# Kernel tuning notes

Hardware: AMD Instinct MI355X
Metric: run time of the kernel (lower is better)

The kernel has to match this reference:

```python
import jax, jax.numpy as jnp
import numpy as np

N, E, F_IN, C, D = 50000, 200000, 384, 384, 16
NEG_SLOPE = 0.2


def setup_inputs() -> dict:
    key = jax.random.key(0)
    ks = jax.random.split(key, 12)
    x = jax.random.normal(ks[0], (N, F_IN), jnp.float32)
    # random edges with no self-loops (PyG GATConv removes self loops before re-adding them)
    src = jax.random.randint(ks[1], (E,), 0, N)
    off = jax.random.randint(ks[2], (E,), 1, N)
    dst = (src + off) % N
    edge_index = jnp.stack([src, dst]).astype(jnp.int32)  # [2, E]
    edge_attr = jax.random.uniform(ks[3], (E, D), jnp.float32)
    # GATConv params (heads=1): lin (no bias), att_src/att_dst/att_edge, lin_edge (no bias), bias
    W_lin = jax.random.normal(ks[4], (F_IN, C), jnp.float32) / np.float32(np.sqrt(F_IN))
    att_src = jax.random.normal(ks[5], (C,), jnp.float32) * 0.1
    att_dst = jax.random.normal(ks[6], (C,), jnp.float32) * 0.1
    W_edge = jax.random.normal(ks[7], (D, C), jnp.float32) / np.float32(np.sqrt(D))
    att_edge = jax.random.normal(ks[8], (C,), jnp.float32) * 0.1
    bias_conv = jnp.zeros((C,), jnp.float32)
    # final Linear(384 -> 1) with bias
    W_out = jax.random.normal(ks[9], (C, 1), jnp.float32) / np.float32(np.sqrt(C))
    b_out = jnp.zeros((1,), jnp.float32)
    return {"x": x, "edge_index": edge_index, "edge_attr": edge_attr,
            "W_lin": W_lin, "att_src": att_src, "att_dst": att_dst,
            "W_edge": W_edge, "att_edge": att_edge, "bias_conv": bias_conv,
            "W_out": W_out, "b_out": b_out}


def _gat_conv(x, edge_index, edge_attr, W_lin, att_src, att_dst, W_edge, att_edge, bias_conv):
    src, dst = edge_index[0], edge_index[1]
    h = x @ W_lin                              # [N, C]
    a_src = h @ att_src                        # [N]
    a_dst = h @ att_dst                        # [N]
    # add self loops; self-loop edge_attr = per-node mean of incoming edge_attr (fill_value='mean')
    deg = jax.ops.segment_sum(jnp.ones((E,), x.dtype), dst, num_segments=N)
    ea_mean = jax.ops.segment_sum(edge_attr, dst, num_segments=N) / jnp.maximum(deg, 1.0)[:, None]
    loop = jnp.arange(N, dtype=src.dtype)
    src_f = jnp.concatenate([src, loop])       # [E+N]
    dst_f = jnp.concatenate([dst, loop])
    ea_f = jnp.concatenate([edge_attr, ea_mean], axis=0)  # [E+N, D]
    a_edge = (ea_f @ W_edge) @ att_edge        # [E+N]
    # per-edge attention logits, segment softmax over destination neighborhoods
    alpha = jax.nn.leaky_relu(a_src[src_f] + a_dst[dst_f] + a_edge, NEG_SLOPE)
    amax = jax.ops.segment_max(alpha, dst_f, num_segments=N)  # every node has a self loop
    ex = jnp.exp(alpha - amax[dst_f])
    denom = jax.ops.segment_sum(ex, dst_f, num_segments=N)
    w = ex / denom[dst_f]                      # [E+N]
    # weighted scatter-aggregate of source messages
    out = jax.ops.segment_sum(h[src_f] * w[:, None], dst_f, num_segments=N)
    return out + bias_conv


def reference(x, edge_index, edge_attr, W_lin, att_src, att_dst, W_edge, att_edge, bias_conv, W_out, b_out):
    h = _gat_conv(x, edge_index, edge_attr, W_lin, att_src, att_dst, W_edge, att_edge, bias_conv)
    return jax.nn.relu(h @ W_out + b_out)      # [N, 1]
```

## Files before the change

### kernel.cpp

```cpp
#include <hip/hip_runtime.h>

#define NEG_SLOPE 0.2f
#define TPB    256
#define NB     256
#define CNT    196
#define EBLK   256
#define PERBLK 32
#define ER     4
#define MAGIC  21913099ULL
#define NBLK2  782

__global__ __launch_bounds__(TPB) void k_fold(
        const float* __restrict__ Wlin, const float* __restrict__ att_src,
        const float* __restrict__ att_dst, const float* __restrict__ Wedge,
        const float* __restrict__ att_edge, const float* __restrict__ bias_conv,
        const float* __restrict__ Wout, const float* __restrict__ bout,
        float* __restrict__ vs, float* __restrict__ va, float* __restrict__ vb,
        float* __restrict__ we, float* __restrict__ cb) {
    const int gwid = (blockIdx.x * TPB + threadIdx.x) >> 6;
    const int lane = threadIdx.x & 63;
    if (gwid < 384) {
        int f = gwid;
        float a = 0.f, b = 0.f, c = 0.f;
        for (int k = lane; k < 384; k += 64) {
            float w = Wlin[f * 384 + k];
            a += w * Wout[k];
            b += w * att_src[k];
            c += w * att_dst[k];
        }
        for (int off = 32; off > 0; off >>= 1) {
            a += __shfl_down(a, off);
            b += __shfl_down(b, off);
            c += __shfl_down(c, off);
        }
        if (lane == 0) { vs[f] = a; va[f] = b; vb[f] = c; }
    } else if (gwid < 400) {
        int d = gwid - 384;
        float a = 0.f;
        for (int k = lane; k < 384; k += 64) a += Wedge[d * 384 + k] * att_edge[k];
        for (int off = 32; off > 0; off >>= 1) a += __shfl_down(a, off);
        if (lane == 0) we[d] = a;
    } else if (gwid == 400) {
        float a = 0.f;
        for (int k = lane; k < 384; k += 64) a += bias_conv[k] * Wout[k];
        for (int off = 32; off > 0; off >>= 1) a += __shfl_down(a, off);
        if (lane == 0) cb[0] = a + bout[0];
    }
}

__global__ __launch_bounds__(TPB) void k_main(
        const float* __restrict__ x,
        const int* __restrict__ src, const int* __restrict__ dst,
        const float* __restrict__ ea,
        const float* __restrict__ vs, const float* __restrict__ va,
        const float* __restrict__ vb, const float* __restrict__ we,
        float* __restrict__ s, float* __restrict__ asrc, float* __restrict__ adst,
        uint2* __restrict__ rec, unsigned int* __restrict__ cnt,
        int N, int E) {
    __shared__ float weL[16];
    __shared__ int   ldsCnt[NB];
    const int tid = threadIdx.x;
    const int blk = blockIdx.x;

    if (blk >= EBLK) {
        const int ll   = tid & 15;
        const int slot = (blk - EBLK) * 16 + (tid >> 4);
        const float4* vs4 = (const float4*)vs;
        const float4* va4 = (const float4*)va;
        const float4* vb4 = (const float4*)vb;
        float4 wsr[6], war[6], wbr[6];
#pragma unroll
        for (int j = 0; j < 6; ++j) {
            wsr[j] = vs4[ll + 16 * j];
            war[j] = va4[ll + 16 * j];
            wbr[j] = vb4[ll + 16 * j];
        }
#pragma unroll
        for (int i = 0; i < 4; ++i) {
            int n = slot + i * (NBLK2 * 16);
            if (n < N) {
                const float4* row = (const float4*)(x + (size_t)n * 384);
                float4 xr[6];
#pragma unroll
                for (int j = 0; j < 6; ++j) xr[j] = row[ll + 16 * j];
                float a = 0.f, b = 0.f, c = 0.f;
#pragma unroll
                for (int j = 0; j < 6; ++j) {
                    a += xr[j].x*wsr[j].x + xr[j].y*wsr[j].y + xr[j].z*wsr[j].z + xr[j].w*wsr[j].w;
                    b += xr[j].x*war[j].x + xr[j].y*war[j].y + xr[j].z*war[j].z + xr[j].w*war[j].w;
                    c += xr[j].x*wbr[j].x + xr[j].y*wbr[j].y + xr[j].z*wbr[j].z + xr[j].w*wbr[j].w;
                }
#pragma unroll
                for (int off = 8; off > 0; off >>= 1) {
                    a += __shfl_xor(a, off);
                    b += __shfl_xor(b, off);
                    c += __shfl_xor(c, off);
                }
                if (ll == 0) { s[n] = a; asrc[n] = b; adst[n] = c; }
            }
        }
        return;
    }

    const int eblk = blk;
    if (tid < 16) weL[tid] = we[tid];
    for (int i = tid; i < NB; i += TPB) ldsCnt[i] = 0;
    __syncthreads();

    const int chunk = (E + EBLK - 1) / EBLK;
    const int ebase = eblk * chunk;
    const int eend  = min(E, ebase + chunk);
    int dnr[ER], rkr[ER], bkr[ER];
#pragma unroll
    for (int r = 0; r < ER; ++r) {
        int e = ebase + r * TPB + tid;
        dnr[r] = -1;
        if (e < eend) {
            int dn = dnr[r] = dst[e];
            int b  = bkr[r] = (int)(((unsigned long long)(unsigned)dn * MAGIC) >> 32);
            rkr[r] = atomicAdd(&ldsCnt[b], 1);
        }
    }
    __syncthreads();
    if (tid < NB) cnt[eblk * NB + tid] = (unsigned)ldsCnt[tid];

    const float4 w0 = make_float4(weL[0],  weL[1],  weL[2],  weL[3]);
    const float4 w1 = make_float4(weL[4],  weL[5],  weL[6],  weL[7]);
    const float4 w2 = make_float4(weL[8],  weL[9],  weL[10], weL[11]);
    const float4 w3 = make_float4(weL[12], weL[13], weL[14], weL[15]);
#pragma unroll
    for (int r = 0; r < ER; ++r) {
        int dn = dnr[r];
        if (dn >= 0 && rkr[r] < PERBLK) {
            int e  = ebase + r * TPB + tid;
            int sn = src[e];
            const float4* rw = (const float4*)(ea + (size_t)e * 16);
            float4 v0 = rw[0], v1 = rw[1], v2 = rw[2], v3 = rw[3];
            float a = v0.x*w0.x + v0.y*w0.y + v0.z*w0.z + v0.w*w0.w
                    + v1.x*w1.x + v1.y*w1.y + v1.z*w1.z + v1.w*w1.w
                    + v2.x*w2.x + v2.y*w2.y + v2.z*w2.z + v2.w*w2.w
                    + v3.x*w3.x + v3.y*w3.y + v3.z*w3.z + v3.w*w3.w;
            int b = bkr[r];
            unsigned key = ((unsigned)(dn - b * CNT) << 16) | (unsigned)sn;
            rec[((size_t)b * EBLK + eblk) * PERBLK + rkr[r]] =
                make_uint2(key, __float_as_uint(a));
        }
    }
}

__global__ __launch_bounds__(TPB) void k_agg(
        const uint2* __restrict__ rec, const unsigned int* __restrict__ cnt,
        const float* __restrict__ asrc, const float* __restrict__ adst,
        const float* __restrict__ s, const float* __restrict__ cb,
        float* __restrict__ out, int n_nodes) {
    __shared__ float4 accL[CNT];
    __shared__ float  adstL[CNT];
    const int b  = blockIdx.x;
    const int lo = b * CNT;
    int cn = n_nodes - lo;
    if (cn <= 0) return;
    if (cn > CNT) cn = CNT;
    const int tid = threadIdx.x;
    for (int r = tid; r < CNT; r += TPB) accL[r] = make_float4(0.f, 0.f, 0.f, 0.f);
    for (int r = tid; r < cn; r += TPB)  adstL[r] = adst[lo + r];
    __syncthreads();
    int m = (int)cnt[tid * NB + b];
    if (m > PERBLK) m = PERBLK;
    const uint2* base = rec + ((size_t)b * EBLK + tid) * PERBLK;
    for (int i = 0; i < m; ++i) {
        uint2 rc = base[i];
        int r  = (int)(rc.x >> 16);
        int sn = (int)(rc.x & 0xFFFFu);
        float a  = __uint_as_float(rc.y);
        float al = asrc[sn] + adstL[r] + a;
        al = al >= 0.f ? al : NEG_SLOPE * al;
        float ex = __expf(al);
        float* bp = (float*)&accL[r];
        atomicAdd(bp + 0, 1.0f);
        atomicAdd(bp + 1, a);
        atomicAdd(bp + 2, ex);
        atomicAdd(bp + 3, ex * s[sn]);
    }
    __syncthreads();
    const float cbv = cb[0];
    for (int r = tid; r < cn; r += TPB) {
        int n = lo + r;
        float4 ac = accL[r];
        float d  = ac.x < 1.f ? 1.f : ac.x;
        float al = asrc[n] + adstL[r] + ac.y / d;
        al = al >= 0.f ? al : NEG_SLOPE * al;
        float ex = __expf(al);
        float v = (ac.w + ex * s[n]) / (ac.z + ex) + cbv;
        out[n] = v > 0.f ? v : 0.f;
    }
}

extern "C" void kernel_launch(void* const* d_in, const int* in_sizes, int n_in,
                              void* d_out, int out_size, void* d_ws, size_t ws_size,
                              hipStream_t stream) {
    const float* x        = (const float*)d_in[0];
    const int*   eidx     = (const int*)d_in[1];
    const float* ea       = (const float*)d_in[2];
    const float* Wlin     = (const float*)d_in[3];
    const float* att_src  = (const float*)d_in[4];
    const float* att_dst  = (const float*)d_in[5];
    const float* Wedge    = (const float*)d_in[6];
    const float* att_edge = (const float*)d_in[7];
    const float* bias_c   = (const float*)d_in[8];
    const float* Wout     = (const float*)d_in[9];
    const float* bout     = (const float*)d_in[10];
    float*       out      = (float*)d_out;

    const int N = in_sizes[0] / 384;
    const int E = in_sizes[2] / 16;
    const int* src = eidx;
    const int* dst = eidx + E;

    float* W = (float*)d_ws;
    float*        vs   = W;
    float*        va   = W + 384;
    float*        vb   = W + 768;
    float*        we   = W + 1152;
    float*        cb   = W + 1168;
    float*        s    = W + 1280;
    float*        asrc = s + N;
    float*        adst = asrc + N;
    unsigned int* cnt  = (unsigned int*)(adst + N);
    uint2*        rec  = (uint2*)(cnt + EBLK * NB);

    k_fold<<<101, TPB, 0, stream>>>(
        Wlin, att_src, att_dst, Wedge, att_edge, bias_c, Wout, bout,
        vs, va, vb, we, cb);
    k_main<<<EBLK + NBLK2, TPB, 0, stream>>>(
        x, src, dst, ea, vs, va, vb, we, s, asrc, adst, rec, cnt, N, E);
    k_agg<<<NB, TPB, 0, stream>>>(
        rec, cnt, asrc, adst, s, cb, out, N);
}
```

Baseline: 35.00 us.

## Restructure node projection to wave-per-8-row tiles with full-wave reductions

The node-projection path of k_main now gives each 64-lane wave a contiguous tile of 8 rows of x. All 12 float4 loads per lane are issued up front and are fully coalesced, and lanes are remapped so that two rows share one 64-lane reduction. This replaces the old 16-lanes-per-row layout with 4 strided rows per group, aiming for more memory-level parallelism and fewer idle lanes on the bandwidth-bound read of x. The change also adds an occupancy hint (launch_bounds min 3 blocks), switches the reductions to xor butterflies, and adds a scalar tail path for a partial final tile. The trade-off is higher register pressure from the 12-deep load buffer and more shuffle steps per row.

```diff
diff --git a/kernel.cpp b/kernel.cpp
--- a/kernel.cpp
+++ b/kernel.cpp
@@ -8,7 +8,12 @@
 #define PERBLK 32
 #define ER     4
 #define MAGIC  21913099ULL
-#define NBLK2  782
+
+__device__ __forceinline__ float wsum64(float v) {
+#pragma unroll
+    for (int off = 1; off < 64; off <<= 1) v += __shfl_xor(v, off);
+    return v;
+}
 
 __global__ __launch_bounds__(TPB) void k_fold(
         const float* __restrict__ Wlin, const float* __restrict__ att_src,
@@ -28,27 +33,23 @@
             b += w * att_src[k];
             c += w * att_dst[k];
         }
-        for (int off = 32; off > 0; off >>= 1) {
-            a += __shfl_down(a, off);
-            b += __shfl_down(b, off);
-            c += __shfl_down(c, off);
-        }
+        a = wsum64(a); b = wsum64(b); c = wsum64(c);
         if (lane == 0) { vs[f] = a; va[f] = b; vb[f] = c; }
     } else if (gwid < 400) {
         int d = gwid - 384;
         float a = 0.f;
         for (int k = lane; k < 384; k += 64) a += Wedge[d * 384 + k] * att_edge[k];
-        for (int off = 32; off > 0; off >>= 1) a += __shfl_down(a, off);
+        a = wsum64(a);
         if (lane == 0) we[d] = a;
     } else if (gwid == 400) {
         float a = 0.f;
         for (int k = lane; k < 384; k += 64) a += bias_conv[k] * Wout[k];
-        for (int off = 32; off > 0; off >>= 1) a += __shfl_down(a, off);
+        a = wsum64(a);
         if (lane == 0) cb[0] = a + bout[0];
     }
 }
 
-__global__ __launch_bounds__(TPB) void k_main(
+__global__ __launch_bounds__(TPB, 3) void k_main(
         const float* __restrict__ x,
         const int* __restrict__ src, const int* __restrict__ dst,
         const float* __restrict__ ea,
@@ -63,40 +64,73 @@
     const int blk = blockIdx.x;
 
     if (blk >= EBLK) {
-        const int ll   = tid & 15;
-        const int slot = (blk - EBLK) * 16 + (tid >> 4);
+        const int lane  = tid & 63;
+        const int wv    = tid >> 6;
+        const int tile  = (blk - EBLK) * 4 + wv;
+        const int row0  = tile * 8;
+        if (row0 >= N) return;
         const float4* vs4 = (const float4*)vs;
         const float4* va4 = (const float4*)va;
         const float4* vb4 = (const float4*)vb;
-        float4 wsr[6], war[6], wbr[6];
-#pragma unroll
-        for (int j = 0; j < 6; ++j) {
-            wsr[j] = vs4[ll + 16 * j];
-            war[j] = va4[ll + 16 * j];
-            wbr[j] = vb4[ll + 16 * j];
-        }
-#pragma unroll
-        for (int i = 0; i < 4; ++i) {
-            int n = slot + i * (NBLK2 * 16);
-            if (n < N) {
-                const float4* row = (const float4*)(x + (size_t)n * 384);
-                float4 xr[6];
-#pragma unroll
-                for (int j = 0; j < 6; ++j) xr[j] = row[ll + 16 * j];
+        const int i0 = lane;
+        const int i1 = lane < 32 ? 64 + lane : lane - 32;
+        const int i2 = 32 + lane;
+        const float4 wS0 = vs4[i0], wS1 = vs4[i1], wS2 = vs4[i2];
+        const float4 wA0 = va4[i0], wA1 = va4[i1], wA2 = va4[i2];
+        const float4 wB0 = vb4[i0], wB1 = vb4[i1], wB2 = vb4[i2];
+
+        if (row0 + 8 <= N) {
+            const float4* t4 = (const float4*)(x + (size_t)row0 * 384);
+            float4 xr[12];
+#pragma unroll
+            for (int r = 0; r < 12; ++r) xr[r] = t4[r * 64 + lane];
+#pragma unroll
+            for (int m = 0; m < 4; ++m) {
+                const float4 x0 = xr[3 * m], x1 = xr[3 * m + 1], x2 = xr[3 * m + 2];
+                float pS0 = x0.x*wS0.x + x0.y*wS0.y + x0.z*wS0.z + x0.w*wS0.w;
+                float pA0 = x0.x*wA0.x + x0.y*wA0.y + x0.z*wA0.z + x0.w*wA0.w;
+                float pB0 = x0.x*wB0.x + x0.y*wB0.y + x0.z*wB0.z + x0.w*wB0.w;
+                float pS1 = x1.x*wS1.x + x1.y*wS1.y + x1.z*wS1.z + x1.w*wS1.w;
+                float pA1 = x1.x*wA1.x + x1.y*wA1.y + x1.z*wA1.z + x1.w*wA1.w;
+                float pB1 = x1.x*wB1.x + x1.y*wB1.y + x1.z*wB1.z + x1.w*wB1.w;
+                float pS2 = x2.x*wS2.x + x2.y*wS2.y + x2.z*wS2.z + x2.w*wS2.w;
+                float pA2 = x2.x*wA2.x + x2.y*wA2.y + x2.z*wA2.z + x2.w*wA2.w;
+                float pB2 = x2.x*wB2.x + x2.y*wB2.y + x2.z*wB2.z + x2.w*wB2.w;
+                const bool loHalf = lane < 32;
+                float rAs = wsum64(pS0 + (loHalf ? pS1 : 0.f));
+                float rAa = wsum64(pA0 + (loHalf ? pA1 : 0.f));
+                float rAb = wsum64(pB0 + (loHalf ? pB1 : 0.f));
+                float rBs = wsum64(pS2 + (loHalf ? 0.f : pS1));
+                float rBa = wsum64(pA2 + (loHalf ? 0.f : pA1));
+                float rBb = wsum64(pB2 + (loHalf ? 0.f : pB1));
+                if (lane == 0) {
+                    int n = row0 + 2 * m;
+                    s[n] = rAs;     asrc[n] = rAa;     adst[n] = rAb;
+                    s[n + 1] = rBs; asrc[n + 1] = rBa; adst[n + 1] = rBb;
+                }
+            }
+        } else {
+            for (int n = row0; n < N; ++n) {
+                const float4* r4 = (const float4*)(x + (size_t)n * 384);
                 float a = 0.f, b = 0.f, c = 0.f;
-#pragma unroll
-                for (int j = 0; j < 6; ++j) {
-                    a += xr[j].x*wsr[j].x + xr[j].y*wsr[j].y + xr[j].z*wsr[j].z + xr[j].w*wsr[j].w;
-                    b += xr[j].x*war[j].x + xr[j].y*war[j].y + xr[j].z*war[j].z + xr[j].w*war[j].w;
-                    c += xr[j].x*wbr[j].x + xr[j].y*wbr[j].y + xr[j].z*wbr[j].z + xr[j].w*wbr[j].w;
+                float4 xv = r4[lane];
+                float4 w  = vs4[lane];
+                a += xv.x*w.x + xv.y*w.y + xv.z*w.z + xv.w*w.w;
+                w = va4[lane];
+                b += xv.x*w.x + xv.y*w.y + xv.z*w.z + xv.w*w.w;
+                w = vb4[lane];
+                c += xv.x*w.x + xv.y*w.y + xv.z*w.z + xv.w*w.w;
+                if (lane < 32) {
+                    xv = r4[64 + lane];
+                    w  = vs4[64 + lane];
+                    a += xv.x*w.x + xv.y*w.y + xv.z*w.z + xv.w*w.w;
+                    w = va4[64 + lane];
+                    b += xv.x*w.x + xv.y*w.y + xv.z*w.z + xv.w*w.w;
+                    w = vb4[64 + lane];
+                    c += xv.x*w.x + xv.y*w.y + xv.z*w.z + xv.w*w.w;
                 }
-#pragma unroll
-                for (int off = 8; off > 0; off >>= 1) {
-                    a += __shfl_xor(a, off);
-                    b += __shfl_xor(b, off);
-                    c += __shfl_xor(c, off);
-                }
-                if (ll == 0) { s[n] = a; asrc[n] = b; adst[n] = c; }
+                a = wsum64(a); b = wsum64(b); c = wsum64(c);
+                if (lane == 0) { s[n] = a; asrc[n] = b; adst[n] = c; }
             }
         }
         return;
@@ -228,10 +262,13 @@
     unsigned int* cnt  = (unsigned int*)(adst + N);
     uint2*        rec  = (uint2*)(cnt + EBLK * NB);
 
+    const int nTiles    = (N + 7) / 8;
+    const int nodeBlks  = (nTiles + 3) / 4;
+
     k_fold<<<101, TPB, 0, stream>>>(
         Wlin, att_src, att_dst, Wedge, att_edge, bias_c, Wout, bout,
         vs, va, vb, we, cb);
-    k_main<<<EBLK + NBLK2, TPB, 0, stream>>>(
+    k_main<<<EBLK + nodeBlks, TPB, 0, stream>>>(
         x, src, dst, ea, vs, va, vb, we, s, asrc, adst, rec, cnt, N, E);
     k_agg<<<NB, TPB, 0, stream>>>(
         rec, cnt, asrc, adst, s, cb, out, N);
```

Result: slower. 36.61 us (+4.6%).

## Stage node feature rows in LDS tiles for projection dot products

Applied to the files above, without the earlier changes.

The node-projection path now has each block copy a tile of 16 rows of x into shared memory with fully coalesced float4 loads. Each wave then computes three dot products per row with a full 64-lane xor reduction. This replaces the old scheme of 16 lanes per row over four strided iterations, so the launch goes from 782 persistent blocks to about 3125 one-tile blocks. It adds a shared-memory round trip, a block barrier and 24KB of LDS per block, including edge blocks, which may lower occupancy. The tail tile copies 16 rows without a bounds check, so it relies on N being divisible by 16.

```diff
diff --git a/kernel.cpp b/kernel.cpp
--- a/kernel.cpp
+++ b/kernel.cpp
@@ -8,7 +8,13 @@
 #define PERBLK 32
 #define ER     4
 #define MAGIC  21913099ULL
-#define NBLK2  782
+#define ROWS   16
+
+__device__ __forceinline__ float wsum64(float v) {
+#pragma unroll
+    for (int off = 1; off < 64; off <<= 1) v += __shfl_xor(v, off);
+    return v;
+}
 
 __global__ __launch_bounds__(TPB) void k_fold(
         const float* __restrict__ Wlin, const float* __restrict__ att_src,
@@ -28,22 +34,18 @@
             b += w * att_src[k];
             c += w * att_dst[k];
         }
-        for (int off = 32; off > 0; off >>= 1) {
-            a += __shfl_down(a, off);
-            b += __shfl_down(b, off);
-            c += __shfl_down(c, off);
-        }
+        a = wsum64(a); b = wsum64(b); c = wsum64(c);
         if (lane == 0) { vs[f] = a; va[f] = b; vb[f] = c; }
     } else if (gwid < 400) {
         int d = gwid - 384;
         float a = 0.f;
         for (int k = lane; k < 384; k += 64) a += Wedge[d * 384 + k] * att_edge[k];
-        for (int off = 32; off > 0; off >>= 1) a += __shfl_down(a, off);
+        a = wsum64(a);
         if (lane == 0) we[d] = a;
     } else if (gwid == 400) {
         float a = 0.f;
         for (int k = lane; k < 384; k += 64) a += bias_conv[k] * Wout[k];
-        for (int off = 32; off > 0; off >>= 1) a += __shfl_down(a, off);
+        a = wsum64(a);
         if (lane == 0) cb[0] = a + bout[0];
     }
 }
@@ -57,46 +59,47 @@
         float* __restrict__ s, float* __restrict__ asrc, float* __restrict__ adst,
         uint2* __restrict__ rec, unsigned int* __restrict__ cnt,
         int N, int E) {
-    __shared__ float weL[16];
-    __shared__ int   ldsCnt[NB];
+    __shared__ float4 xtile[ROWS * 96];
+    __shared__ float  weL[16];
+    __shared__ int    ldsCnt[NB];
     const int tid = threadIdx.x;
     const int blk = blockIdx.x;
 
     if (blk >= EBLK) {
-        const int ll   = tid & 15;
-        const int slot = (blk - EBLK) * 16 + (tid >> 4);
+        const int tile = blk - EBLK;
+        const int row0 = tile * ROWS;
+        if (row0 >= N) return;
+        const float4* x4 = (const float4*)x + (size_t)row0 * 96;
+#pragma unroll
+        for (int k = 0; k < 6; ++k) {
+            int f4i = tid + k * TPB;
+            xtile[f4i] = x4[f4i];
+        }
+        __syncthreads();
+        const int lane = tid & 63;
+        const int wv   = tid >> 6;
         const float4* vs4 = (const float4*)vs;
         const float4* va4 = (const float4*)va;
         const float4* vb4 = (const float4*)vb;
-        float4 wsr[6], war[6], wbr[6];
-#pragma unroll
-        for (int j = 0; j < 6; ++j) {
-            wsr[j] = vs4[ll + 16 * j];
-            war[j] = va4[ll + 16 * j];
-            wbr[j] = vb4[ll + 16 * j];
-        }
-#pragma unroll
-        for (int i = 0; i < 4; ++i) {
-            int n = slot + i * (NBLK2 * 16);
-            if (n < N) {
-                const float4* row = (const float4*)(x + (size_t)n * 384);
-                float4 xr[6];
-#pragma unroll
-                for (int j = 0; j < 6; ++j) xr[j] = row[ll + 16 * j];
-                float a = 0.f, b = 0.f, c = 0.f;
-#pragma unroll
-                for (int j = 0; j < 6; ++j) {
-                    a += xr[j].x*wsr[j].x + xr[j].y*wsr[j].y + xr[j].z*wsr[j].z + xr[j].w*wsr[j].w;
-                    b += xr[j].x*war[j].x + xr[j].y*war[j].y + xr[j].z*war[j].z + xr[j].w*war[j].w;
-                    c += xr[j].x*wbr[j].x + xr[j].y*wbr[j].y + xr[j].z*wbr[j].z + xr[j].w*wbr[j].w;
-                }
-#pragma unroll
-                for (int off = 8; off > 0; off >>= 1) {
-                    a += __shfl_xor(a, off);
-                    b += __shfl_xor(b, off);
-                    c += __shfl_xor(c, off);
-                }
-                if (ll == 0) { s[n] = a; asrc[n] = b; adst[n] = c; }
+        const int i1 = 64 + (lane & 31);
+        const float4 wS0 = vs4[lane], wS1 = vs4[i1];
+        const float4 wA0 = va4[lane], wA1 = va4[i1];
+        const float4 wB0 = vb4[lane], wB1 = vb4[i1];
+        const float m1 = (lane < 32) ? 1.f : 0.f;
+#pragma unroll
+        for (int r = wv * 4; r < wv * 4 + 4; ++r) {
+            const float4 x0 = xtile[r * 96 + lane];
+            const float4 x1 = xtile[r * 96 + i1];
+            float a = x0.x*wS0.x + x0.y*wS0.y + x0.z*wS0.z + x0.w*wS0.w
+                    + m1 * (x1.x*wS1.x + x1.y*wS1.y + x1.z*wS1.z + x1.w*wS1.w);
+            float b = x0.x*wA0.x + x0.y*wA0.y + x0.z*wA0.z + x0.w*wA0.w
+                    + m1 * (x1.x*wA1.x + x1.y*wA1.y + x1.z*wA1.z + x1.w*wA1.w);
+            float c = x0.x*wB0.x + x0.y*wB0.y + x0.z*wB0.z + x0.w*wB0.w
+                    + m1 * (x1.x*wB1.x + x1.y*wB1.y + x1.z*wB1.z + x1.w*wB1.w);
+            a = wsum64(a); b = wsum64(b); c = wsum64(c);
+            if (lane == 0) {
+                int n = row0 + r;
+                s[n] = a; asrc[n] = b; adst[n] = c;
             }
         }
         return;
@@ -228,10 +231,12 @@
     unsigned int* cnt  = (unsigned int*)(adst + N);
     uint2*        rec  = (uint2*)(cnt + EBLK * NB);
 
+    const int nodeBlks = (N + ROWS - 1) / ROWS;
+
     k_fold<<<101, TPB, 0, stream>>>(
         Wlin, att_src, att_dst, Wedge, att_edge, bias_c, Wout, bout,
         vs, va, vb, we, cb);
-    k_main<<<EBLK + NBLK2, TPB, 0, stream>>>(
+    k_main<<<EBLK + nodeBlks, TPB, 0, stream>>>(
         x, src, dst, ea, vs, va, vb, we, s, asrc, adst, rec, cnt, N, E);
     k_agg<<<NB, TPB, 0, stream>>>(
         rec, cnt, asrc, adst, s, cb, out, N);
```

Result: slower. 37.56 us (+7.3%).
